# Kernel tuning notes

Measured on AMD Instinct MI355X. Metric: run time of the kernel, lower is better.

The kernel has to match this reference:

```python
import jax, jax.numpy as jnp
import numpy as np

N_NODES = 100000
D = 50            # node embedding dim; concat -> in_dim = 2*D = 100
N_EDGES = 2000000
HIDDEN = 32


def setup_inputs() -> dict:
    key = jax.random.key(0)
    k_z, k_e, k_w1, k_w2 = jax.random.split(key, 4)
    z = jax.random.normal(k_z, (N_NODES, D), dtype=jnp.float32)
    edge_label_index = jax.random.randint(k_e, (2, N_EDGES), 0, N_NODES, dtype=jnp.int64)
    # Linear params (stored as [in, out] for x @ W + b)
    W1 = jax.random.normal(k_w1, (2 * D, HIDDEN), dtype=jnp.float32) * (1.0 / np.sqrt(2 * D))
    b1 = jnp.zeros((HIDDEN,), dtype=jnp.float32)
    W2 = jax.random.normal(k_w2, (HIDDEN, 1), dtype=jnp.float32) * (1.0 / np.sqrt(HIDDEN))
    b2 = jnp.zeros((1,), dtype=jnp.float32)
    return {"z": z, "edge_label_index": edge_label_index,
            "W1": W1, "b1": b1, "W2": W2, "b2": b2}


def reference(z, edge_label_index, W1, b1, W2, b2):
    # Gather src/dst node embeddings: [E, D] each
    src = z[edge_label_index[0]]
    dst = z[edge_label_index[1]]
    x = jnp.concatenate([src, dst], axis=1)          # [E, 2D]
    h = jax.nn.relu(x @ W1 + b1)                      # [E, HIDDEN]; dropout is identity in eval
    out = h @ W2 + b2                                 # [E, 1]
    return out.reshape(-1)                            # [E]
```

## Files before the change

### kernel.cpp

```cpp
#include <hip/hip_runtime.h>
#include <hip/hip_fp16.h>

#define D 50
#define HIDDEN 32
#define NPN 32

__device__ __forceinline__ float proj_dot(float zv, const float* Breg, float bias) {
    float acc = bias;
#pragma unroll
    for (int k = 0; k < D; ++k) {
        float zk = __uint_as_float(
            (unsigned)__builtin_amdgcn_readlane((int)__float_as_uint(zv), k));
        acc = fmaf(zk, Breg[k], acc);
    }
    return acc;
}

__device__ __forceinline__ void store_row(__half2* __restrict__ P2, int n,
                                          int lane, float acc) {
    float nb = __shfl_xor(acc, 1);
    if ((lane & 1) == 0) {
        P2[(size_t)n * 32 + (lane >> 1)] = __floats2half2_rn(acc, nb);
    }
}

__global__ __launch_bounds__(256, 4) void node_proj_kernel(
        const float* __restrict__ z,
        const float* __restrict__ W1,
        const float* __restrict__ b1,
        __half2* __restrict__ P2,
        int n_nodes) {
    const int lane = threadIdx.x & 63;
    const int wid  = (blockIdx.x * blockDim.x + threadIdx.x) >> 6;

    int n0 = wid * NPN;
    if (n0 >= n_nodes) return;
    int nend = n0 + NPN;
    if (nend > n_nodes) nend = n_nodes;

    const int j    = lane & 31;
    const int half = lane >> 5;

    float Breg[D];
    const float* wcol = W1 + (size_t)(half * D) * HIDDEN + j;
#pragma unroll
    for (int k = 0; k < D; ++k) Breg[k] = wcol[(size_t)k * HIDDEN];

    const float bias = half ? 0.0f : b1[j];
    const bool  ld   = (lane < D);

    for (int n = n0; n < nend; n += 4) {
        int rem = nend - n;
        float zv0 = ld            ? z[(size_t)n * D + lane]       : 0.0f;
        float zv1 = (ld && rem > 1) ? z[(size_t)(n + 1) * D + lane] : 0.0f;
        float zv2 = (ld && rem > 2) ? z[(size_t)(n + 2) * D + lane] : 0.0f;
        float zv3 = (ld && rem > 3) ? z[(size_t)(n + 3) * D + lane] : 0.0f;

        store_row(P2, n, lane, proj_dot(zv0, Breg, bias));
        if (rem > 1) store_row(P2, n + 1, lane, proj_dot(zv1, Breg, bias));
        if (rem > 2) store_row(P2, n + 2, lane, proj_dot(zv2, Breg, bias));
        if (rem > 3) store_row(P2, n + 3, lane, proj_dot(zv3, Breg, bias));
    }
}

__global__ void edge_mlp_kernel(const int* __restrict__ eidx,
                                const __half* __restrict__ P,
                                const float* __restrict__ W2,
                                const float* __restrict__ b2,
                                float* __restrict__ out,
                                int n_edges) {
    int t = blockIdx.x * blockDim.x + threadIdx.x;
    int e = t >> 2;
    int r = t & 3;
    if (e >= n_edges) return;

    int s = eidx[e];
    int d = eidx[n_edges + e];

    uint4 ua = *(const uint4*)(P + (size_t)s * 64 + r * 8);
    uint4 ub = *(const uint4*)(P + (size_t)d * 64 + 32 + r * 8);
    float4 w0 = *(const float4*)(W2 + r * 8);
    float4 w1 = *(const float4*)(W2 + r * 8 + 4);

    float2 a0 = __half22float2(*(const __half2*)&ua.x);
    float2 a1 = __half22float2(*(const __half2*)&ua.y);
    float2 a2 = __half22float2(*(const __half2*)&ua.z);
    float2 a3 = __half22float2(*(const __half2*)&ua.w);
    float2 b0 = __half22float2(*(const __half2*)&ub.x);
    float2 b1v = __half22float2(*(const __half2*)&ub.y);
    float2 b2v = __half22float2(*(const __half2*)&ub.z);
    float2 b3 = __half22float2(*(const __half2*)&ub.w);

    float acc = (r == 0) ? b2[0] : 0.0f;
    acc = fmaf(fmaxf(a0.x + b0.x,  0.0f), w0.x, acc);
    acc = fmaf(fmaxf(a0.y + b0.y,  0.0f), w0.y, acc);
    acc = fmaf(fmaxf(a1.x + b1v.x, 0.0f), w0.z, acc);
    acc = fmaf(fmaxf(a1.y + b1v.y, 0.0f), w0.w, acc);
    acc = fmaf(fmaxf(a2.x + b2v.x, 0.0f), w1.x, acc);
    acc = fmaf(fmaxf(a2.y + b2v.y, 0.0f), w1.y, acc);
    acc = fmaf(fmaxf(a3.x + b3.x,  0.0f), w1.z, acc);
    acc = fmaf(fmaxf(a3.y + b3.y,  0.0f), w1.w, acc);

    acc += __shfl_xor(acc, 1);
    acc += __shfl_xor(acc, 2);

    if (r == 0) out[e] = acc;
}

__global__ void edge_direct_kernel(const float* __restrict__ z,
                                   const int* __restrict__ eidx,
                                   const float* __restrict__ W1,
                                   const float* __restrict__ b1,
                                   const float* __restrict__ W2,
                                   const float* __restrict__ b2,
                                   float* __restrict__ out,
                                   int n_edges) {
    int e = blockIdx.x * blockDim.x + threadIdx.x;
    if (e >= n_edges) return;
    int s = eidx[e];
    int d = eidx[n_edges + e];
    const float* zs = z + (size_t)s * D;
    const float* zd = z + (size_t)d * D;
    float acc = b2[0];
    for (int j = 0; j < HIDDEN; ++j) {
        float h = b1[j];
        for (int k = 0; k < D; ++k) {
            h = fmaf(zs[k], W1[(size_t)k * HIDDEN + j], h);
            h = fmaf(zd[k], W1[(size_t)(D + k) * HIDDEN + j], h);
        }
        acc = fmaf(fmaxf(h, 0.0f), W2[j], acc);
    }
    out[e] = acc;
}

extern "C" void kernel_launch(void* const* d_in, const int* in_sizes, int n_in,
                              void* d_out, int out_size, void* d_ws, size_t ws_size,
                              hipStream_t stream) {
    const float* z    = (const float*)d_in[0];
    const int*   eidx = (const int*)d_in[1];
    const float* W1   = (const float*)d_in[2];
    const float* b1   = (const float*)d_in[3];
    const float* W2   = (const float*)d_in[4];
    const float* b2   = (const float*)d_in[5];
    float*       out  = (float*)d_out;

    const int n_nodes = in_sizes[0] / D;
    const int n_edges = in_sizes[1] / 2;

    const size_t p_bytes = (size_t)n_nodes * 64 * sizeof(__half);

    if (p_bytes <= ws_size) {
        __half* P = (__half*)d_ws;

        int n_waves = (n_nodes + NPN - 1) / NPN;
        int blocks1 = (n_waves * 64 + 255) / 256;
        node_proj_kernel<<<blocks1, 256, 0, stream>>>(z, W1, b1, (__half2*)P,
                                                      n_nodes);

        long long total2 = (long long)n_edges * 4;
        int blocks2 = (int)((total2 + 255) / 256);
        edge_mlp_kernel<<<blocks2, 256, 0, stream>>>(eidx, P, W2, b2, out, n_edges);
    } else {
        int blocks = (n_edges + 255) / 256;
        edge_direct_kernel<<<blocks, 256, 0, stream>>>(z, eidx, W1, b1, W2, b2,
                                                       out, n_edges);
    }
}
```

Baseline: 89.05 us.

## Compute node projection with bf16 MFMA using prepacked weight fragments

The scalar readlane-based per-node projection is replaced by a bf16 MFMA 16x16x32 kernel that handles 16-node tiles. A small pre-kernel packs W1 and b1 into bf16 B-fragments, with the bias folded in through a constant-1 input column. This removes the long serial FMA chains in the projection stage, which is small next to the edge gather kernel. In exchange z and W1 are rounded to bf16, which lowers precision, and there is one extra launch.

```diff
diff --git a/kernel.cpp b/kernel.cpp
--- a/kernel.cpp
+++ b/kernel.cpp
@@ -3,63 +3,112 @@
 
 #define D 50
 #define HIDDEN 32
-#define NPN 32
-
-__device__ __forceinline__ float proj_dot(float zv, const float* Breg, float bias) {
-    float acc = bias;
-#pragma unroll
-    for (int k = 0; k < D; ++k) {
-        float zk = __uint_as_float(
-            (unsigned)__builtin_amdgcn_readlane((int)__float_as_uint(zv), k));
-        acc = fmaf(zk, Breg[k], acc);
-    }
-    return acc;
-}
-
-__device__ __forceinline__ void store_row(__half2* __restrict__ P2, int n,
-                                          int lane, float acc) {
-    float nb = __shfl_xor(acc, 1);
-    if ((lane & 1) == 0) {
-        P2[(size_t)n * 32 + (lane >> 1)] = __floats2half2_rn(acc, nb);
-    }
-}
-
-__global__ __launch_bounds__(256, 4) void node_proj_kernel(
+#define TPW 2
+
+using short8 = __attribute__((ext_vector_type(8))) short;
+using f32x4  = __attribute__((ext_vector_type(4))) float;
+
+static __device__ __forceinline__ short bfbits(float f) {
+    unsigned u = __float_as_uint(f);
+    unsigned r = (u + 0x7FFFu + ((u >> 16) & 1u)) >> 16;
+    return (short)r;
+}
+
+__global__ void build_w1tb_kernel(const float* __restrict__ W1,
+                                  const float* __restrict__ b1,
+                                  short* __restrict__ W1TB) {
+    int idx = blockIdx.x * blockDim.x + threadIdx.x;
+    if (idx >= 512) return;
+    int f  = idx >> 6;
+    int l  = idx & 63;
+    int jt = f >> 1, ks = f & 1;
+    int kg = l >> 4,  c = l & 15;
+    int j  = jt * 16 + c;
+
+    short v[8];
+#pragma unroll
+    for (int e = 0; e < 8; ++e) {
+        int k = ks * 32 + kg * 8 + e;
+        float x = 0.0f;
+        if (k < D)       x = (j < 32) ? W1[(size_t)k * HIDDEN + j]
+                                      : W1[(size_t)(D + k) * HIDDEN + (j - 32)];
+        else if (k == D) x = (j < 32) ? b1[j] : 0.0f;
+        v[e] = bfbits(x);
+    }
+    int4 o;
+    o.x = (v[1] << 16) | (v[0] & 0xffff);
+    o.y = (v[3] << 16) | (v[2] & 0xffff);
+    o.z = (v[5] << 16) | (v[4] & 0xffff);
+    o.w = (v[7] << 16) | (v[6] & 0xffff);
+    *(int4*)(W1TB + (size_t)f * 512 + l * 8) = o;
+}
+
+__global__ __launch_bounds__(256) void node_proj_mfma_kernel(
         const float* __restrict__ z,
-        const float* __restrict__ W1,
-        const float* __restrict__ b1,
+        const short* __restrict__ W1TB,
         __half2* __restrict__ P2,
         int n_nodes) {
     const int lane = threadIdx.x & 63;
     const int wid  = (blockIdx.x * blockDim.x + threadIdx.x) >> 6;
-
-    int n0 = wid * NPN;
-    if (n0 >= n_nodes) return;
-    int nend = n0 + NPN;
-    if (nend > n_nodes) nend = n_nodes;
-
-    const int j    = lane & 31;
-    const int half = lane >> 5;
-
-    float Breg[D];
-    const float* wcol = W1 + (size_t)(half * D) * HIDDEN + j;
-#pragma unroll
-    for (int k = 0; k < D; ++k) Breg[k] = wcol[(size_t)k * HIDDEN];
-
-    const float bias = half ? 0.0f : b1[j];
-    const bool  ld   = (lane < D);
-
-    for (int n = n0; n < nend; n += 4) {
-        int rem = nend - n;
-        float zv0 = ld            ? z[(size_t)n * D + lane]       : 0.0f;
-        float zv1 = (ld && rem > 1) ? z[(size_t)(n + 1) * D + lane] : 0.0f;
-        float zv2 = (ld && rem > 2) ? z[(size_t)(n + 2) * D + lane] : 0.0f;
-        float zv3 = (ld && rem > 3) ? z[(size_t)(n + 3) * D + lane] : 0.0f;
-
-        store_row(P2, n, lane, proj_dot(zv0, Breg, bias));
-        if (rem > 1) store_row(P2, n + 1, lane, proj_dot(zv1, Breg, bias));
-        if (rem > 2) store_row(P2, n + 2, lane, proj_dot(zv2, Breg, bias));
-        if (rem > 3) store_row(P2, n + 3, lane, proj_dot(zv3, Breg, bias));
+    const int kg   = lane >> 4;
+    const int c    = lane & 15;
+
+    short8 bf[8];
+#pragma unroll
+    for (int f = 0; f < 8; ++f)
+        bf[f] = *(const short8*)(W1TB + (size_t)f * 512 + lane * 8);
+
+    for (int t = 0; t < TPW; ++t) {
+        int tile = wid * TPW + t;
+        int nb   = tile * 16;
+        if (nb >= n_nodes) return;
+
+        int  rown = nb + c;
+        bool rv   = rown < n_nodes;
+        const float* zrow = z + (size_t)(rv ? rown : 0) * D;
+
+        float za[8], zb[8];
+        {
+            const float2* p = (const float2*)(zrow + kg * 8);
+            float2 q0 = p[0], q1 = p[1], q2 = p[2], q3 = p[3];
+            za[0] = q0.x; za[1] = q0.y; za[2] = q1.x; za[3] = q1.y;
+            za[4] = q2.x; za[5] = q2.y; za[6] = q3.x; za[7] = q3.y;
+        }
+        if (kg < 2) {
+            const float2* p = (const float2*)(zrow + 32 + kg * 8);
+            float2 q0 = p[0], q1 = p[1], q2 = p[2], q3 = p[3];
+            zb[0] = q0.x; zb[1] = q0.y; zb[2] = q1.x; zb[3] = q1.y;
+            zb[4] = q2.x; zb[5] = q2.y; zb[6] = q3.x; zb[7] = q3.y;
+        } else if (kg == 2) {
+            float2 q0 = *(const float2*)(zrow + 48);
+            zb[0] = q0.x; zb[1] = q0.y;
+            zb[2] = 1.0f;
+            zb[3] = zb[4] = zb[5] = zb[6] = zb[7] = 0.0f;
+        } else {
+#pragma unroll
+            for (int e = 0; e < 8; ++e) zb[e] = 0.0f;
+        }
+
+        short8 a0, a1;
+#pragma unroll
+        for (int e = 0; e < 8; ++e) { a0[e] = bfbits(za[e]); a1[e] = bfbits(zb[e]); }
+
+#pragma unroll
+        for (int jt = 0; jt < 4; ++jt) {
+            f32x4 acc = {0.0f, 0.0f, 0.0f, 0.0f};
+            acc = __builtin_amdgcn_mfma_f32_16x16x32_bf16(a0, bf[jt * 2],     acc, 0, 0, 0);
+            acc = __builtin_amdgcn_mfma_f32_16x16x32_bf16(a1, bf[jt * 2 + 1], acc, 0, 0, 0);
+#pragma unroll
+            for (int r = 0; r < 4; ++r) {
+                float v0 = acc[r];
+                float v1 = __shfl_xor(v0, 1);
+                int node = nb + kg * 4 + r;
+                if (((lane & 1) == 0) && node < n_nodes) {
+                    P2[(size_t)node * 32 + jt * 8 + (c >> 1)] =
+                        __floats2half2_rn(v0, v1);
+                }
+            }
+        }
     }
 }
 
@@ -148,14 +197,19 @@
     const int n_edges = in_sizes[1] / 2;
 
     const size_t p_bytes = (size_t)n_nodes * 64 * sizeof(__half);
-
-    if (p_bytes <= ws_size) {
-        __half* P = (__half*)d_ws;
-
-        int n_waves = (n_nodes + NPN - 1) / NPN;
-        int blocks1 = (n_waves * 64 + 255) / 256;
-        node_proj_kernel<<<blocks1, 256, 0, stream>>>(z, W1, b1, (__half2*)P,
-                                                      n_nodes);
+    const size_t w_bytes = (size_t)8 * 512 * sizeof(short);
+
+    if (p_bytes + w_bytes <= ws_size) {
+        __half* P    = (__half*)d_ws;
+        short*  W1TB = (short*)((char*)d_ws + p_bytes);
+
+        build_w1tb_kernel<<<2, 256, 0, stream>>>(W1, b1, W1TB);
+
+        int tiles   = (n_nodes + 15) / 16;
+        int waves   = (tiles + TPW - 1) / TPW;
+        int blocks1 = (waves * 64 + 255) / 256;
+        node_proj_mfma_kernel<<<blocks1, 256, 0, stream>>>(z, W1TB, (__half2*)P,
+                                                           n_nodes);
 
         long long total2 = (long long)n_edges * 4;
         int blocks2 = (int)((total2 + 255) / 256);
```

Measured after the change: 71.40 us. -19.8%, faster.
